# Performance work log

Measured on AMD Instinct MI355X. Metric: run time of the kernel, lower is better.

Reference implementation:

```python
import jax, jax.numpy as jnp
import numpy as np
from jax.scipy.special import logsumexp

D_MODEL = 512
NHEAD = 8
BATCH = 2
SEQ = 1024


def _safe_log_relu(v):
    # log(max(v, 0)) with well-defined (zero) gradient where v <= 0
    pos = v > 0
    return jnp.where(pos, jnp.log(jnp.where(pos, v, 1.0)), -jnp.inf)


def _split_heads(t, h):
    b, l, hd = t.shape
    return t.reshape(b, l, h, hd // h).transpose(0, 2, 1, 3)  # (B,H,L,d)


def setup_inputs() -> dict:
    key = jax.random.key(0)
    ks = jax.random.split(key, 9)
    s = 1.0 / np.sqrt(D_MODEL)
    x = jax.random.normal(ks[0], (BATCH, SEQ, D_MODEL), jnp.float32)
    mk = lambda k: jax.random.normal(k, (D_MODEL, D_MODEL), jnp.float32) * s
    mb = lambda k: jax.random.normal(k, (D_MODEL,), jnp.float32) * 0.02
    return {
        "x": x,
        "W_Q": mk(ks[1]), "b_Q": mb(ks[2]),
        "W_K": mk(ks[3]), "b_K": mb(ks[4]),
        "W_V": mk(ks[5]), "b_V": mb(ks[6]),
        "W_O": mk(ks[7]), "b_O": mb(ks[8]),
    }


def reference(x, W_Q, b_Q, W_K, b_K, W_V, b_V, W_O, b_O):
    # self-attention: queries = keys = values = x
    Q = _split_heads(x @ W_Q.T + b_Q, NHEAD)  # (B,H,L,D)
    K = _split_heads(x @ W_K.T + b_K, NHEAD)  # (B,H,L,D)
    V = _split_heads(x @ W_V.T + b_V, NHEAD)  # (B,H,L,Dv)

    # normalizer: log sum_j sum_d exp(Q_id) * exp(K_jd)
    log_B = logsumexp(Q + logsumexp(K, axis=-2, keepdims=True), axis=-1)  # (B,H,L)

    log_V_plus = _safe_log_relu(V)[..., None, :]    # (B,H,L,1,Dv)
    log_V_minus = _safe_log_relu(-V)[..., None, :]  # (B,H,L,1,Dv)

    # reduce over key positions: (B,H,L,D,Dv) -> (B,H,D,Dv)
    lse_KV_plus = logsumexp(K[..., :, :, None] + log_V_plus, axis=-3)
    lse_KV_minus = logsumexp(K[..., :, :, None] + log_V_minus, axis=-3)

    # reduce over feature dim D: (B,H,L,D,Dv) -> (B,H,L,Dv)
    log_A_plus = logsumexp(Q[..., None] + lse_KV_plus[..., None, :, :], axis=-2)
    log_A_minus = logsumexp(Q[..., None] + lse_KV_minus[..., None, :, :], axis=-2)

    heads = jnp.exp(log_A_plus - log_B[..., None]) - jnp.exp(log_A_minus - log_B[..., None])

    b, h, l, dv = heads.shape
    joined = heads.transpose(0, 2, 1, 3).reshape(b, l, h * dv)
    return joined @ W_O.T + b_O
```

## Files before the change

### kernel.cpp

```cpp
#include <hip/hip_runtime.h>
#include <math.h>

#define DM   512
#define NH   8
#define HD   64
#define B_   2
#define L_   1024
#define M_   (B_ * L_)

typedef __attribute__((ext_vector_type(8))) short  bfrag;
typedef __attribute__((ext_vector_type(4))) float  fv4;
typedef __attribute__((ext_vector_type(4))) unsigned short usv4;
typedef __attribute__((ext_vector_type(8))) unsigned short usv8;

__device__ __forceinline__ unsigned short f32_bf16_rne(float f) {
    unsigned u = __float_as_uint(f);
    unsigned r = u + 0x7FFF + ((u >> 16) & 1);
    return (unsigned short)(r >> 16);
}
__device__ __forceinline__ float bf16_f32(unsigned short h) {
    return __uint_as_float(((unsigned)h) << 16);
}

__device__ __forceinline__ void stage16(const unsigned short* g, unsigned short* l) {
    __builtin_amdgcn_global_load_lds(
        (const __attribute__((address_space(1))) void*)g,
        (__attribute__((address_space(3))) void*)l,
        16, 0, 0);
}

__global__ __launch_bounds__(256) void prep_kernel(
    const float* __restrict__ x,
    const float* __restrict__ Wq, const float* __restrict__ Wk,
    const float* __restrict__ Wv,
    unsigned short* __restrict__ xh, unsigned short* __restrict__ xl,
    unsigned short* __restrict__ wh, unsigned short* __restrict__ wl,
    float* __restrict__ zred) {
    int bid = blockIdx.x;
    if (bid >= 1792) {
        float4 zv = {0.f, 0.f, 0.f, 0.f};
        *(float4*)(zred + (size_t)threadIdx.x * 4) = zv;
        return;
    }
    const float* src; unsigned short *dh, *dl; size_t off;
    if (bid < 1024) {
        src = x; dh = xh; dl = xl; off = (size_t)bid * 1024;
    } else {
        int wsel = (bid - 1024) >> 8;
        int wb   = (bid - 1024) & 255;
        src = (wsel == 0) ? Wq : (wsel == 1) ? Wk : Wv;
        dh = wh + (size_t)wsel * 262144;
        dl = wl + (size_t)wsel * 262144;
        off = (size_t)wb * 1024;
    }
    size_t i = off + (size_t)threadIdx.x * 4;
    float4 v = *(const float4*)(src + i);
    usv4 h, l;
    h.x = f32_bf16_rne(v.x); l.x = f32_bf16_rne(v.x - bf16_f32(h.x));
    h.y = f32_bf16_rne(v.y); l.y = f32_bf16_rne(v.y - bf16_f32(h.y));
    h.z = f32_bf16_rne(v.z); l.z = f32_bf16_rne(v.z - bf16_f32(h.z));
    h.w = f32_bf16_rne(v.w); l.w = f32_bf16_rne(v.w - bf16_f32(h.w));
    *(usv4*)(dh + i) = h;
    *(usv4*)(dl + i) = l;
}

#define TM 128
#define TN 64
#define TK 32
#define LDA 32

__device__ __forceinline__ void mfma_gemm_bf16(
    const unsigned short* __restrict__ Ahg, const unsigned short* __restrict__ Alg,
    const unsigned short* __restrict__ Bhg, const unsigned short* __restrict__ Blg,
    const float* __restrict__ bias, float* __restrict__ C, int do_exp) {
    __shared__ __align__(16) unsigned short Ah[TM * LDA];
    __shared__ __align__(16) unsigned short Al[TM * LDA];
    __shared__ __align__(16) unsigned short Bh[TN * LDA];
    __shared__ __align__(16) unsigned short Bl[TN * LDA];

    const int tid  = threadIdx.x;
    const int wave = tid >> 6, lane = tid & 63;
    const int quad = lane >> 4, r16 = lane & 15;
    const int m0 = blockIdx.y * TM, n0 = blockIdx.x * TN;

    const int srow = lane >> 2;
    const int scol = (lane & 3) << 3;

    fv4 acc[2][4] = {};

    for (int k0 = 0; k0 < DM; k0 += TK) {
        {
            const int c1 = wave, c2 = wave + 4;
            size_t ga1 = (size_t)(m0 + c1 * 16 + srow) * DM + k0 + scol;
            size_t ga2 = (size_t)(m0 + c2 * 16 + srow) * DM + k0 + scol;
            stage16(Ahg + ga1, Ah + c1 * 512);
            stage16(Ahg + ga2, Ah + c2 * 512);
            stage16(Alg + ga1, Al + c1 * 512);
            stage16(Alg + ga2, Al + c2 * 512);
            size_t gb = (size_t)(n0 + c1 * 16 + srow) * DM + k0 + scol;
            stage16(Bhg + gb, Bh + c1 * 512);
            stage16(Blg + gb, Bl + c1 * 512);
        }
        __syncthreads();

        bfrag ah[2], al[2], bh[4], bl[4];
#pragma unroll
        for (int i = 0; i < 2; ++i) {
            int off = (wave * 32 + i * 16 + r16) * LDA + quad * 8;
            ah[i] = *(const bfrag*)(Ah + off);
            al[i] = *(const bfrag*)(Al + off);
        }
#pragma unroll
        for (int j = 0; j < 4; ++j) {
            int off = (j * 16 + r16) * LDA + quad * 8;
            bh[j] = *(const bfrag*)(Bh + off);
            bl[j] = *(const bfrag*)(Bl + off);
        }

#pragma unroll
        for (int i = 0; i < 2; ++i)
#pragma unroll
            for (int j = 0; j < 4; ++j) {
                acc[i][j] = __builtin_amdgcn_mfma_f32_16x16x32_bf16(ah[i], bh[j], acc[i][j], 0, 0, 0);
                acc[i][j] = __builtin_amdgcn_mfma_f32_16x16x32_bf16(ah[i], bl[j], acc[i][j], 0, 0, 0);
                acc[i][j] = __builtin_amdgcn_mfma_f32_16x16x32_bf16(al[i], bh[j], acc[i][j], 0, 0, 0);
            }
        __syncthreads();
    }

#pragma unroll
    for (int j = 0; j < 4; ++j) {
        int n = n0 + j * 16 + r16;
        float bn = bias[n];
#pragma unroll
        for (int i = 0; i < 2; ++i) {
#pragma unroll
            for (int r = 0; r < 4; ++r) {
                int m = m0 + wave * 32 + i * 16 + quad * 4 + r;
                float v = acc[i][j][r] + bn;
                if (do_exp) v = __expf(v);
                C[(size_t)m * DM + n] = v;
            }
        }
    }
}

__global__ __launch_bounds__(256) void gemm_qkv_kernel(
    const unsigned short* __restrict__ xh, const unsigned short* __restrict__ xl,
    const unsigned short* __restrict__ wh, const unsigned short* __restrict__ wl,
    const float* __restrict__ bq, const float* __restrict__ bk, const float* __restrict__ bv,
    float* __restrict__ Qe, float* __restrict__ Ke, float* __restrict__ V) {
    int z = blockIdx.z;
    const float* b = (z == 0) ? bq : (z == 1) ? bk : bv;
    float* C = (z == 0) ? Qe : (z == 1) ? Ke : V;
    mfma_gemm_bf16(xh, xl, wh + (size_t)z * 262144, wl + (size_t)z * 262144,
                   b, C, z < 2);
}

__global__ __launch_bounds__(256) void gemm_out_kernel(
    const unsigned short* __restrict__ jh, const unsigned short* __restrict__ jl,
    const unsigned short* __restrict__ w2h, const unsigned short* __restrict__ w2l,
    const float* __restrict__ bo, float* __restrict__ C) {
    int b = blockIdx.y >> 3;
    mfma_gemm_bf16(jh, jl, w2h + (size_t)b * 262144, w2l + (size_t)b * 262144,
                   bo, C, 0);
}

#define JT 64
__global__ __launch_bounds__(256) void kv_stats_kernel(
    const float* __restrict__ Kbuf, const float* __restrict__ Vbuf,
    float* __restrict__ Spart, float* __restrict__ zred) {
    const int split = blockIdx.x, bh = blockIdx.y;
    const int b = bh >> 3, h = bh & 7;
    const int j0 = split * JT;

    __shared__ __align__(16) float EK[JT][HD + 4];
    __shared__ __align__(16) float VS[JT][HD + 4];

    const int tid = threadIdx.x;
#pragma unroll
    for (int t = 0; t < 4; ++t) {
        int idx = tid + t * 256;
        int r = idx >> 4;
        int c = (idx & 15) << 2;
        size_t row = (size_t)(b * L_ + j0 + r) * DM + h * HD + c;
        *(float4*)&EK[r][c] = *(const float4*)(Kbuf + row);
        *(float4*)&VS[r][c] = *(const float4*)(Vbuf + row);
    }
    __syncthreads();

    const int tx = tid & 15, ty = tid >> 4;
    float acc[4][4] = {{0.f}};
#pragma unroll 8
    for (int jj = 0; jj < JT; ++jj) {
        float4 ek = *(const float4*)&EK[jj][ty * 4];
        float4 vs = *(const float4*)&VS[jj][tx * 4];
        float e[4] = {ek.x, ek.y, ek.z, ek.w};
        float v[4] = {vs.x, vs.y, vs.z, vs.w};
#pragma unroll
        for (int i = 0; i < 4; ++i)
#pragma unroll
            for (int j = 0; j < 4; ++j) acc[i][j] += e[i] * v[j];
    }

    float* sp = Spart + ((size_t)bh * 16 + split) * (HD * HD);
#pragma unroll
    for (int i = 0; i < 4; ++i) {
        float4 o; o.x = acc[i][0]; o.y = acc[i][1]; o.z = acc[i][2]; o.w = acc[i][3];
        *(float4*)(sp + (ty * 4 + i) * HD + tx * 4) = o;
    }
    if (tid < HD) {
        float z = 0.f;
#pragma unroll 8
        for (int jj = 0; jj < JT; ++jj) z += EK[jj][tid];
        atomicAdd(zred + (size_t)bh * HD + tid, z);
    }
}

__global__ __launch_bounds__(256) void mid_kernel(
    const float* __restrict__ Spart, const float* __restrict__ zred,
    const float* __restrict__ Qbuf, const float* __restrict__ Wo,
    unsigned short* __restrict__ w2h, unsigned short* __restrict__ w2l,
    unsigned short* __restrict__ jh, unsigned short* __restrict__ jl) {
    const int tid = threadIdx.x;
    const int bid = blockIdx.x;
    if (bid < 128) {
        __shared__ __align__(16) float Sl[HD][HD + 4];
        __shared__ __align__(16) float Wol[HD][HD + 4];
        const int b = bid >> 6, r = bid & 63;
        const int h = r >> 3, nq = r & 7;
        const int n0 = nq * 64, bh = b * NH + h;
        const float* sp = Spart + (size_t)bh * 16 * (HD * HD);
#pragma unroll
        for (int t4 = 0; t4 < 4; ++t4) {
            int idx4 = tid + t4 * 256;
            const float* p0 = sp + (size_t)idx4 * 4;
            float4 s = {0.f, 0.f, 0.f, 0.f};
#pragma unroll
            for (int p = 0; p < 16; ++p) {
                float4 v = *(const float4*)(p0 + (size_t)p * (HD * HD));
                s.x += v.x; s.y += v.y; s.z += v.z; s.w += v.w;
            }
            int d = idx4 >> 4, e4 = (idx4 & 15) << 2;
            *(float4*)&Sl[d][e4] = s;
            *(float4*)&Wol[d][e4] =
                *(const float4*)(Wo + (size_t)(n0 + d) * DM + h * HD + e4);
        }
        __syncthreads();
        const int nl = tid & 15;
        const int d0 = tid >> 4;
        float acc[4][4] = {};
#pragma unroll
        for (int e4 = 0; e4 < 16; ++e4) {
            float4 w[4], s[4];
#pragma unroll
            for (int j = 0; j < 4; ++j) w[j] = *(const float4*)&Wol[nl + j * 16][e4 * 4];
#pragma unroll
            for (int i = 0; i < 4; ++i) s[i] = *(const float4*)&Sl[d0 + i * 16][e4 * 4];
#pragma unroll
            for (int j = 0; j < 4; ++j)
#pragma unroll
                for (int i = 0; i < 4; ++i)
                    acc[j][i] += w[j].x * s[i].x + w[j].y * s[i].y
                               + w[j].z * s[i].z + w[j].w * s[i].w;
        }
#pragma unroll
        for (int j = 0; j < 4; ++j) {
            int n = n0 + nl + j * 16;
#pragma unroll
            for (int i = 0; i < 4; ++i) {
                int d = d0 + i * 16;
                size_t addr = ((size_t)(b * DM + n)) * DM + h * HD + d;
                float v = acc[j][i];
                unsigned short hh = f32_bf16_rne(v);
                w2h[addr] = hh;
                w2l[addr] = f32_bf16_rne(v - bf16_f32(hh));
            }
        }
    } else {
        const int bid2 = bid - 128;
        const int w = tid >> 6, lane = tid & 63;
        const int b = bid2 >> 5;
        const int row0 = bid2 * 32 + w * 8;
        const float4 z0 = *(const float4*)(zred + (size_t)b * DM + lane * 8);
        const float4 z1 = *(const float4*)(zred + (size_t)b * DM + lane * 8 + 4);
#pragma unroll
        for (int rr = 0; rr < 8; ++rr) {
            const size_t rowoff = (size_t)(row0 + rr) * DM + lane * 8;
            float4 q0 = *(const float4*)(Qbuf + rowoff);
            float4 q1 = *(const float4*)(Qbuf + rowoff + 4);
            float part = q0.x * z0.x + q0.y * z0.y + q0.z * z0.z + q0.w * z0.w
                       + q1.x * z1.x + q1.y * z1.y + q1.z * z1.z + q1.w * z1.w;
            part += __shfl_xor(part, 1, 64);
            part += __shfl_xor(part, 2, 64);
            part += __shfl_xor(part, 4, 64);
            float inv = 1.0f / part;
            float v[8] = {q0.x * inv, q0.y * inv, q0.z * inv, q0.w * inv,
                          q1.x * inv, q1.y * inv, q1.z * inv, q1.w * inv};
            usv8 hv, lv;
#pragma unroll
            for (int k = 0; k < 8; ++k) {
                unsigned short hh = f32_bf16_rne(v[k]);
                hv[k] = hh;
                lv[k] = f32_bf16_rne(v[k] - bf16_f32(hh));
            }
            *(usv8*)(jh + rowoff) = hv;
            *(usv8*)(jl + rowoff) = lv;
        }
    }
}

extern "C" void kernel_launch(void* const* d_in, const int* in_sizes, int n_in,
                              void* d_out, int out_size, void* d_ws, size_t ws_size,
                              hipStream_t stream) {
    const float* x  = (const float*)d_in[0];
    const float* Wq = (const float*)d_in[1];
    const float* bq = (const float*)d_in[2];
    const float* Wk = (const float*)d_in[3];
    const float* bk = (const float*)d_in[4];
    const float* Wv = (const float*)d_in[5];
    const float* bv = (const float*)d_in[6];
    const float* Wo = (const float*)d_in[7];
    const float* bo = (const float*)d_in[8];
    float* out = (float*)d_out;

    float* f = (float*)d_ws;
    const size_t NQ = (size_t)M_ * DM;
    float* Qe    = f;
    float* Ke    = f + NQ;
    float* V     = f + 2 * NQ;
    float* Spart = f + 3 * NQ;
    float* zred  = f + 4 * NQ;
    unsigned short* u = (unsigned short*)(f + 4 * NQ + 1024);
    unsigned short* xh  = u;
    unsigned short* xl  = u + NQ;
    unsigned short* wh  = u + 2 * NQ;
    unsigned short* wl  = u + 2 * NQ + 786432;
    unsigned short* jh  = u + 2 * NQ + 2 * 786432;
    unsigned short* jl  = jh + NQ;
    unsigned short* w2h = jl + NQ;
    unsigned short* w2l = w2h + 524288;

    prep_kernel<<<1793, 256, 0, stream>>>(x, Wq, Wk, Wv, xh, xl, wh, wl, zred);

    dim3 gQKV(DM / TN, M_ / TM, 3);
    gemm_qkv_kernel<<<gQKV, 256, 0, stream>>>(xh, xl, wh, wl, bq, bk, bv, Qe, Ke, V);

    kv_stats_kernel<<<dim3(16, 16), 256, 0, stream>>>(Ke, V, Spart, zred);

    mid_kernel<<<192, 256, 0, stream>>>(Spart, zred, Qe, Wo, w2h, w2l, jh, jl);

    dim3 gO(DM / TN, M_ / TM, 1);
    gemm_out_kernel<<<gO, 256, 0, stream>>>(jh, jl, w2h, w2l, bo, out);
}
```

Before: 130.6 us.

## Halve GEMM M-tile and double-buffer LDS staging in MFMA GEMM

The bf16 split-precision MFMA GEMM now uses 64-row tiles instead of 128, so each wave owns one 16-row strip and the launch has twice as many blocks. Shared-memory staging becomes ping-pong double-buffered: the next K-slice is loaded while the current one feeds the MFMAs, leaving one barrier per step. The aim is to fill more CUs on these small projection GEMMs and to hide global-load latency. In exchange, each block reuses B data less and LDS use per block doubles. The output kernel's batch index is updated for the new tile height; the grid must also use the new tile height.

```diff
diff --git a/kernel.cpp b/kernel.cpp
--- a/kernel.cpp
+++ b/kernel.cpp
@@ -64,68 +64,67 @@
     *(usv4*)(dl + i) = l;
 }
 
-#define TM 128
+#define TM 64
 #define TN 64
 #define TK 32
 #define LDA 32
+#define NSTEP (DM / TK)
 
 __device__ __forceinline__ void mfma_gemm_bf16(
     const unsigned short* __restrict__ Ahg, const unsigned short* __restrict__ Alg,
     const unsigned short* __restrict__ Bhg, const unsigned short* __restrict__ Blg,
-    const float* __restrict__ bias, float* __restrict__ C, int do_exp) {
-    __shared__ __align__(16) unsigned short Ah[TM * LDA];
-    __shared__ __align__(16) unsigned short Al[TM * LDA];
-    __shared__ __align__(16) unsigned short Bh[TN * LDA];
-    __shared__ __align__(16) unsigned short Bl[TN * LDA];
+    const float* __restrict__ bias, float* __restrict__ C, int do_exp,
+    int m0, int n0) {
+    __shared__ __align__(16) unsigned short Ah[2][TM * LDA];
+    __shared__ __align__(16) unsigned short Al[2][TM * LDA];
+    __shared__ __align__(16) unsigned short Bh[2][TN * LDA];
+    __shared__ __align__(16) unsigned short Bl[2][TN * LDA];
 
     const int tid  = threadIdx.x;
     const int wave = tid >> 6, lane = tid & 63;
     const int quad = lane >> 4, r16 = lane & 15;
-    const int m0 = blockIdx.y * TM, n0 = blockIdx.x * TN;
 
     const int srow = lane >> 2;
     const int scol = (lane & 3) << 3;
-
-    fv4 acc[2][4] = {};
-
-    for (int k0 = 0; k0 < DM; k0 += TK) {
-        {
-            const int c1 = wave, c2 = wave + 4;
-            size_t ga1 = (size_t)(m0 + c1 * 16 + srow) * DM + k0 + scol;
-            size_t ga2 = (size_t)(m0 + c2 * 16 + srow) * DM + k0 + scol;
-            stage16(Ahg + ga1, Ah + c1 * 512);
-            stage16(Ahg + ga2, Ah + c2 * 512);
-            stage16(Alg + ga1, Al + c1 * 512);
-            stage16(Alg + ga2, Al + c2 * 512);
-            size_t gb = (size_t)(n0 + c1 * 16 + srow) * DM + k0 + scol;
-            stage16(Bhg + gb, Bh + c1 * 512);
-            stage16(Blg + gb, Bl + c1 * 512);
+    const size_t gaBase = (size_t)(m0 + wave * 16 + srow) * DM + scol;
+    const size_t gbBase = (size_t)(n0 + wave * 16 + srow) * DM + scol;
+    const int ldst = wave * 512;
+
+    fv4 acc[4] = {};
+
+    stage16(Ahg + gaBase, &Ah[0][ldst]);
+    stage16(Alg + gaBase, &Al[0][ldst]);
+    stage16(Bhg + gbBase, &Bh[0][ldst]);
+    stage16(Blg + gbBase, &Bl[0][ldst]);
+    __syncthreads();
+
+    int cur = 0;
+    for (int t = 0; t < NSTEP; ++t) {
+        if (t + 1 < NSTEP) {
+            const size_t koff = (size_t)(t + 1) * TK;
+            stage16(Ahg + gaBase + koff, &Ah[cur ^ 1][ldst]);
+            stage16(Alg + gaBase + koff, &Al[cur ^ 1][ldst]);
+            stage16(Bhg + gbBase + koff, &Bh[cur ^ 1][ldst]);
+            stage16(Blg + gbBase + koff, &Bl[cur ^ 1][ldst]);
+        }
+        const int aoff = (wave * 16 + r16) * LDA + quad * 8;
+        bfrag ah = *(const bfrag*)(&Ah[cur][aoff]);
+        bfrag al = *(const bfrag*)(&Al[cur][aoff]);
+        bfrag bh[4], bl[4];
+#pragma unroll
+        for (int j = 0; j < 4; ++j) {
+            const int boff = (j * 16 + r16) * LDA + quad * 8;
+            bh[j] = *(const bfrag*)(&Bh[cur][boff]);
+            bl[j] = *(const bfrag*)(&Bl[cur][boff]);
+        }
+#pragma unroll
+        for (int j = 0; j < 4; ++j) {
+            acc[j] = __builtin_amdgcn_mfma_f32_16x16x32_bf16(ah, bh[j], acc[j], 0, 0, 0);
+            acc[j] = __builtin_amdgcn_mfma_f32_16x16x32_bf16(ah, bl[j], acc[j], 0, 0, 0);
+            acc[j] = __builtin_amdgcn_mfma_f32_16x16x32_bf16(al, bh[j], acc[j], 0, 0, 0);
         }
         __syncthreads();
-
-        bfrag ah[2], al[2], bh[4], bl[4];
-#pragma unroll
-        for (int i = 0; i < 2; ++i) {
-            int off = (wave * 32 + i * 16 + r16) * LDA + quad * 8;
-            ah[i] = *(const bfrag*)(Ah + off);
-            al[i] = *(const bfrag*)(Al + off);
-        }
-#pragma unroll
-        for (int j = 0; j < 4; ++j) {
-            int off = (j * 16 + r16) * LDA + quad * 8;
-            bh[j] = *(const bfrag*)(Bh + off);
-            bl[j] = *(const bfrag*)(Bl + off);
-        }
-
-#pragma unroll
-        for (int i = 0; i < 2; ++i)
-#pragma unroll
-            for (int j = 0; j < 4; ++j) {
-                acc[i][j] = __builtin_amdgcn_mfma_f32_16x16x32_bf16(ah[i], bh[j], acc[i][j], 0, 0, 0);
-                acc[i][j] = __builtin_amdgcn_mfma_f32_16x16x32_bf16(ah[i], bl[j], acc[i][j], 0, 0, 0);
-                acc[i][j] = __builtin_amdgcn_mfma_f32_16x16x32_bf16(al[i], bh[j], acc[i][j], 0, 0, 0);
-            }
-        __syncthreads();
+        cur ^= 1;
     }
 
 #pragma unroll
@@ -133,14 +132,11 @@
         int n = n0 + j * 16 + r16;
         float bn = bias[n];
 #pragma unroll
-        for (int i = 0; i < 2; ++i) {
-#pragma unroll
-            for (int r = 0; r < 4; ++r) {
-                int m = m0 + wave * 32 + i * 16 + quad * 4 + r;
-                float v = acc[i][j][r] + bn;
-                if (do_exp) v = __expf(v);
-                C[(size_t)m * DM + n] = v;
-            }
+        for (int r = 0; r < 4; ++r) {
+            int m = m0 + wave * 16 + quad * 4 + r;
+            float v = acc[j][r] + bn;
+            if (do_exp) v = __expf(v);
+            C[(size_t)m * DM + n] = v;
         }
     }
 }
@@ -154,16 +150,16 @@
     const float* b = (z == 0) ? bq : (z == 1) ? bk : bv;
     float* C = (z == 0) ? Qe : (z == 1) ? Ke : V;
     mfma_gemm_bf16(xh, xl, wh + (size_t)z * 262144, wl + (size_t)z * 262144,
-                   b, C, z < 2);
+                   b, C, z < 2, blockIdx.y * TM, blockIdx.x * TN);
 }
 
 __global__ __launch_bounds__(256) void gemm_out_kernel(
     const unsigned short* __restrict__ jh, const unsigned short* __restrict__ jl,
     const unsigned short* __restrict__ w2h, const unsigned short* __restrict__ w2l,
     const float* __restrict__ bo, float* __restrict__ C) {
-    int b = blockIdx.y >> 3;
+    int b = blockIdx.y >> 4;
     mfma_gemm_bf16(jh, jl, w2h + (size_t)b * 262144, w2l + (size_t)b * 262144,
-                   bo, C, 0);
+                   bo, C, 0, blockIdx.y * TM, blockIdx.x * TN);
 }
 
 #define JT 64
```

Measured after the change: 131.3 us. No clear change (+0.5%).
